# Kernel optimization log

Hardware: AMD Instinct MI355X
Metric: run time of the kernel (lower is better)

The kernel has to match this reference:

```python
import jax, jax.numpy as jnp
import numpy as np
from math import sqrt

NUM_ENT = 100000
NUM_REL = 237  # base; rel table has 2*NUM_REL rows
DIM = 200
HALF = DIM // 2


def _lrelu(x, slope):
    return jnp.where(x >= 0, x, slope * x)


def setup_inputs() -> dict:
    key = jax.random.key(0)
    ks = jax.random.split(key, 20)
    s = 0.02
    inp = {
        'edge_index': jax.random.randint(ks[0], (2, 500000), 0, NUM_ENT),
        'edge_type': jax.random.randint(ks[1], (500000,), 0, 2 * NUM_REL),
        'toTest': jax.random.randint(ks[2], (131072, 2), 0, NUM_ENT),
        'ent_emb': s * jax.random.normal(ks[3], (NUM_ENT, DIM), jnp.float32),
        'rel_emb': s * jax.random.normal(ks[4], (2 * NUM_REL, DIM), jnp.float32),
        'W': s * jax.random.normal(ks[5], (DIM, DIM), jnp.float32),
        'W_loop': s * jax.random.normal(ks[6], (DIM, DIM), jnp.float32),
        'W_rel': s * jax.random.normal(ks[7], (DIM, DIM), jnp.float32),
        'trans_w': s * jax.random.normal(ks[8], (DIM, HALF), jnp.float32),
        'trans_b': jnp.zeros((HALF,), jnp.float32),
        'q_w': s * jax.random.normal(ks[9], (HALF, 128), jnp.float32),
        'q_b': jnp.zeros((128,), jnp.float32),
        'k_w': s * jax.random.normal(ks[10], (HALF, 128), jnp.float32),
        'k_b': jnp.zeros((128,), jnp.float32),
        'w1': s * jax.random.normal(ks[11], (DIM * 2 + 1 + 2 * NUM_REL, 2048), jnp.float32),
        'b1': jnp.zeros((2048,), jnp.float32),
        'w2': s * jax.random.normal(ks[12], (2048, 512), jnp.float32),
        'b2': jnp.zeros((512,), jnp.float32),
        'w3': s * jax.random.normal(ks[13], (512, 1), jnp.float32),
        'b3': jnp.zeros((1,), jnp.float32),
    }
    return inp


def reference(ent_emb, rel_emb, W, W_loop, W_rel, trans_w, trans_b,
              q_w, q_b, k_w, k_b, w1, b1, w2, b2, w3, b3,
              edge_index, edge_type, toTest):
    # --- CompGCN base layer ('sub' composition, degree-normalized scatter-add) ---
    src, dst = edge_index[0], edge_index[1]
    msg = (ent_emb[src] - rel_emb[edge_type]) @ W          # [E, D] gather + GEMM
    deg = jax.ops.segment_sum(jnp.ones_like(dst, jnp.float32), dst, num_segments=NUM_ENT)
    norm = jax.lax.rsqrt(jnp.maximum(deg, 1.0))
    agg = jax.ops.segment_sum(msg, dst, num_segments=NUM_ENT) * norm[:, None]
    all_ent = jnp.tanh(agg + ent_emb @ W_loop)             # [num_ent, D]
    all_rel = rel_emb @ W_rel                              # [2*num_rel, D]

    # --- PairRE test scoring path ---
    head_rel = all_rel[:, :HALF]                           # [2R, D/2]
    tail_rel = all_rel[:, HALF:]
    te = all_ent[toTest]                                   # [N, 2, D] gather
    ee = te @ trans_w + trans_b                            # [N, 2, D/2]
    h_e, t_e = ee[:, 0], ee[:, 1]
    atta = ((h_e @ q_w + q_b) * (t_e @ k_w + k_b)).sum(-1, keepdims=True) / sqrt(DIM)
    relSim = h_e @ head_rel.T - t_e @ tail_rel.T           # [N, 2R]
    cat = jnp.concatenate([te[:, 0], te[:, 1], atta, relSim], axis=1)
    h1 = _lrelu(cat @ w1 + b1, 1e-4)
    h2 = _lrelu(h1 @ w2 + b2, 1e-3)
    return jax.nn.sigmoid(h2 @ w3 + b3)                    # [N, 1]
```

## Files before the change

kernel.cpp:

```cpp
#include <hip/hip_runtime.h>

typedef unsigned short u16;
typedef unsigned long long u64;
typedef __attribute__((ext_vector_type(8))) short bf8;
typedef __attribute__((ext_vector_type(4))) float fx4;

#define N_ENT   100000
#define N_EDGE  500000
#define N_TEST  131072
#define EDIM    200
#define AE_LD   224
#define NB_SCAN 391

__device__ __forceinline__ u16 f2bf(float f) {
  union { float f; unsigned u; } c; c.f = f;
  return (u16)((c.u + 0x7FFFu + ((c.u >> 16) & 1u)) >> 16);
}
__device__ __forceinline__ float bf2f(u16 h) {
  union { unsigned u; float f; } c; c.u = ((unsigned)h) << 16;
  return c.f;
}
__device__ __forceinline__ void gload16(const u16* g, u16* l) {
  __builtin_amdgcn_global_load_lds(
      (const __attribute__((address_space(1))) void*)g,
      (__attribute__((address_space(3))) void*)l, 16, 0, 0);
}

#define BK 32
#define EPS 72

template<int TM, int WN>
__global__ __launch_bounds__(64 * 2 * WN) void gemm_t(
    const u16* __restrict__ A, long lda,
    const u16* __restrict__ B, long ldb,
    u16* __restrict__ out, long ldOut,
    int K,
    const int* __restrict__ rowIdx, int idxMode, int mClamp,
    int mValid, int nValid, int nStore,
    const float* __restrict__ bias, int act, float slope,
    const u16* __restrict__ qbuf, const float* __restrict__ auxF,
    float* __restrict__ dotOut)
{
  constexpr int BM = TM * 32;
  constexpr int BN = WN * 64;
  constexpr int WAVES = 2 * WN;
  __shared__ __align__(16) u16 smem[WAVES * 32 * EPS];
  u16* As = smem;
  u16* Bs = smem + BM * BK;
  const int tid  = threadIdx.x;
  const int wave = tid >> 6, lane = tid & 63;
  const int wr = (wave / WN) * (TM * 16), wc = (wave % WN) * 64;
  const int fr = lane & 15, fq = lane >> 4;
  const long bm = (long)blockIdx.x * BM, bn = (long)blockIdx.y * BN;

  const int srow = wave * 32;
  const int kc = (((lane & 3) ^ ((lane >> 3) & 3)) * 8);
  long a0[2], a1[2], boff[2];
  #pragma unroll
  for (int h = 0; h < 2; ++h) {
    long gmRow = bm + srow + h * 16 + (lane >> 2);
    long b0, b1;
    if (idxMode == 0) {
      long gm = (gmRow >= mClamp) ? (mClamp - 1) : gmRow;
      b0 = gm * lda; b1 = b0;
    } else if (idxMode == 2) {
      b0 = (long)rowIdx[2 * gmRow] * lda; b1 = b0;
    } else if (idxMode == 3) {
      b0 = (long)rowIdx[2 * gmRow + 1] * lda; b1 = b0;
    } else {
      b0 = (long)rowIdx[2 * gmRow] * lda;
      b1 = (long)rowIdx[2 * gmRow + 1] * lda - 224;
    }
    a0[h] = b0 + kc; a1[h] = b1 + kc;
    boff[h] = (bn + srow + h * 16 + (lane >> 2)) * ldb + kc;
  }

  fx4 zero4 = {0.f, 0.f, 0.f, 0.f};
  fx4 acc[TM][4];
  #pragma unroll
  for (int i = 0; i < TM; ++i)
    #pragma unroll
    for (int j = 0; j < 4; ++j) acc[i][j] = zero4;

  for (int k0 = 0; k0 < K; k0 += BK) {
    __syncthreads();
    const bool lo = (k0 + kc) < 224;
    #pragma unroll
    for (int h = 0; h < 2; ++h) {
      const long ao = (idxMode == 4) ? (lo ? a0[h] : a1[h]) : a0[h];
      gload16(A + ao + k0, &As[(srow + h * 16) * BK]);
      gload16(B + boff[h] + k0, &Bs[(srow + h * 16) * BK]);
    }
    __syncthreads();
    bf8 aF[TM], bF[4];
    const int rslot = (fq ^ ((fr >> 1) & 3)) * 8;
    #pragma unroll
    for (int mt = 0; mt < TM; ++mt)
      aF[mt] = *(const bf8*)&As[(wr + mt * 16 + fr) * BK + rslot];
    #pragma unroll
    for (int nt = 0; nt < 4; ++nt)
      bF[nt] = *(const bf8*)&Bs[(wc + nt * 16 + fr) * BK + rslot];
    #pragma unroll
    for (int mt = 0; mt < TM; ++mt)
      #pragma unroll
      for (int nt = 0; nt < 4; ++nt)
        acc[mt][nt] = __builtin_amdgcn_mfma_f32_16x16x32_bf16(aF[mt], bF[nt], acc[mt][nt], 0, 0, 0);
  }

  if (act == 3 || act == 4) {
    #pragma unroll
    for (int mt = 0; mt < TM; ++mt) {
      #pragma unroll
      for (int r = 0; r < 4; ++r) {
        const long gm = bm + wr + mt * 16 + fq * 4 + r;
        float p = 0.f;
        #pragma unroll
        for (int nt = 0; nt < 4; ++nt) {
          const long gn = bn + wc + nt * 16 + fr;
          float v = acc[mt][nt][r] + bias[gn];
          if (act == 3) p += v * bf2f(qbuf[gm * 128 + gn]);
          else { v = (v >= 0.f) ? v : v * slope; p += v * auxF[gn]; }
        }
        p += __shfl_xor(p, 1, 64); p += __shfl_xor(p, 2, 64);
        p += __shfl_xor(p, 4, 64); p += __shfl_xor(p, 8, 64);
        if (fr == 0 && gm < mValid)
          atomicAdd(&dotOut[gm], (act == 3) ? p * 0.07071067811865475f : p);
      }
    }
    return;
  }

  __syncthreads();
  u16* ep = smem + wave * (32 * EPS);
  #pragma unroll
  for (int p = 0; p < TM / 2; ++p) {
    #pragma unroll
    for (int mt2 = 0; mt2 < 2; ++mt2) {
      const int mt = 2 * p + mt2;
      #pragma unroll
      for (int r = 0; r < 4; ++r) {
        const int lrl = mt2 * 16 + fq * 4 + r;
        const long gm = bm + wr + mt * 16 + fq * 4 + r;
        const float attaV = (act == 5) ? dotOut[gm] : 0.f;
        #pragma unroll
        for (int nt = 0; nt < 4; ++nt) {
          const long gn = bn + wc + nt * 16 + fr;
          float v = 0.f;
          if (gn < nValid) {
            v = acc[mt][nt][r];
            if (bias) v += bias[gn];
            if (act == 1) v = tanhf(v);
            else if (act == 5) { v += attaV * auxF[gn]; v = (v >= 0.f) ? v : v * slope; }
          }
          ep[lrl * EPS + nt * 16 + fr] = f2bf(v);
        }
      }
    }
    #pragma unroll
    for (int it = 0; it < 4; ++it) {
      const int lr = it * 8 + (lane >> 3);
      const int lc = (lane & 7) * 8;
      const long gm = bm + wr + p * 32 + lr;
      const long gn = bn + wc + lc;
      if (gm < mValid && gn + 7 < nStore)
        *(bf8*)(out + gm * ldOut + gn) = *(const bf8*)&ep[lr * EPS + lc];
    }
  }
}

__global__ void hist_kernel(const int* __restrict__ ei, int* __restrict__ cnt) {
  int e = blockIdx.x * 256 + threadIdx.x;
  if (e < N_EDGE) atomicAdd(&cnt[ei[N_EDGE + e]], 1);
}
__global__ void scanA_kernel(const int* __restrict__ cnt, int* __restrict__ offs,
                             int* __restrict__ blockSums) {
  __shared__ int s[256];
  int gid = blockIdx.x * 256 + threadIdx.x;
  int v = (gid < N_ENT) ? cnt[gid] : 0;
  s[threadIdx.x] = v;
  __syncthreads();
  for (int off = 1; off < 256; off <<= 1) {
    int t = (threadIdx.x >= off) ? s[threadIdx.x - off] : 0;
    __syncthreads();
    s[threadIdx.x] += t;
    __syncthreads();
  }
  if (gid < N_ENT) offs[gid] = s[threadIdx.x] - v;
  if (threadIdx.x == 255) blockSums[blockIdx.x] = s[255];
}
__global__ void scanB_kernel(const int* __restrict__ blockSums, int* __restrict__ blockOffs) {
  __shared__ int s[512];
  int v = (threadIdx.x < NB_SCAN) ? blockSums[threadIdx.x] : 0;
  s[threadIdx.x] = v;
  __syncthreads();
  for (int off = 1; off < 512; off <<= 1) {
    int t = (threadIdx.x >= off) ? s[threadIdx.x - off] : 0;
    __syncthreads();
    s[threadIdx.x] += t;
    __syncthreads();
  }
  if (threadIdx.x < NB_SCAN) blockOffs[threadIdx.x] = s[threadIdx.x] - v;
}
__global__ void scanC_kernel(int* __restrict__ offs, const int* __restrict__ blockOffs) {
  int gid = blockIdx.x * 256 + threadIdx.x;
  if (gid < N_ENT) offs[gid] += blockOffs[blockIdx.x];
}
__global__ void place_kernel(const int* __restrict__ ei, const int* __restrict__ et,
                             const int* __restrict__ offs, int* __restrict__ cursor,
                             int* __restrict__ sortedSrc, int* __restrict__ sortedT) {
  int e = blockIdx.x * 256 + threadIdx.x;
  if (e >= N_EDGE) return;
  int dst = ei[N_EDGE + e];
  int pos = offs[dst] + atomicAdd(&cursor[dst], 1);
  sortedSrc[pos] = ei[e];
  sortedT[pos]   = et[e];
}
__global__ void agg_A1_kernel(const int* __restrict__ offs, const int* __restrict__ cnt,
                              const int* __restrict__ sortedSrc, const int* __restrict__ sortedT,
                              const float* __restrict__ ent_emb, const float* __restrict__ rel_emb,
                              u16* __restrict__ A1) {
  const int r = blockIdx.x * 4 + (threadIdx.x >> 6);
  if (r >= N_ENT) return;
  const int lane = threadIdx.x & 63;
  const int beg = offs[r], n = cnt[r];
  u16* row = A1 + (size_t)r * 416;
  if (lane < 50) {
    float4 a = {0.f, 0.f, 0.f, 0.f};
    for (int e = 0; e < n; ++e) {
      const int s = sortedSrc[beg + e], t = sortedT[beg + e];
      float4 x = ((const float4*)(ent_emb + (size_t)s * EDIM))[lane];
      float4 y = ((const float4*)(rel_emb + (size_t)t * EDIM))[lane];
      a.x += x.x - y.x; a.y += x.y - y.y; a.z += x.z - y.z; a.w += x.w - y.w;
    }
    const float nm = rsqrtf(fmaxf((float)n, 1.f));
    u64 p = (u64)f2bf(a.x * nm) | ((u64)f2bf(a.y * nm) << 16)
          | ((u64)f2bf(a.z * nm) << 32) | ((u64)f2bf(a.w * nm) << 48);
    *(u64*)(row + 4 * lane) = p;
    float4 e = ((const float4*)(ent_emb + (size_t)r * EDIM))[lane];
    u64 q = (u64)f2bf(e.x) | ((u64)f2bf(e.y) << 16)
          | ((u64)f2bf(e.z) << 32) | ((u64)f2bf(e.w) << 48);
    *(u64*)(row + 200 + 4 * lane) = q;
  }
  if (lane < 16) row[400 + lane] = 0;
}

__global__ void build_B1T(const float* __restrict__ W, const float* __restrict__ W_loop,
                          u16* __restrict__ B1T)
{
  int idx = blockIdx.x * 256 + threadIdx.x;
  if (idx >= 256 * 416) return;
  int n = idx / 416, k = idx % 416;
  float v = 0.f;
  if (n < 200) {
    if (k < 200) v = W[k * 200 + n];
    else if (k < 400) v = W_loop[(k - 200) * 200 + n];
  }
  B1T[idx] = f2bf(v);
}
__global__ void all_rel_kernel(const float* __restrict__ rel_emb, const float* __restrict__ W_rel,
                               float* __restrict__ all_rel)
{
  int r = blockIdx.x, c = threadIdx.x;
  if (c >= 200) return;
  const float* re = rel_emb + r * 200;
  float a = 0.f;
  for (int k = 0; k < 200; ++k) a += re[k] * W_rel[k * 200 + c];
  all_rel[r * 200 + c] = a;
}
__global__ void pq_kernel(const float* __restrict__ all_rel, const float* __restrict__ w1,
                          float* __restrict__ PQ) {
  int idx = blockIdx.x * 256 + threadIdx.x;
  if (idx >= 2 * 100 * 2048) return;
  int n = idx & 2047, m = (idx >> 11) % 100, sel = idx / 204800;
  float a = 0.f;
  for (int r = 0; r < 474; ++r)
    a += all_rel[r * 200 + sel * 100 + m] * w1[(size_t)(401 + r) * 2048 + n];
  PQ[idx] = a;
}
__global__ void p2_kernel(const float* __restrict__ trans_w, const float* __restrict__ PQ,
                          float* __restrict__ P2) {
  int idx = blockIdx.x * 256 + threadIdx.x;
  if (idx >= 2 * 200 * 2048) return;
  int n = idx & 2047, k = (idx >> 11) % 200, sel = idx / 409600;
  const float* pq = PQ + sel * 204800;
  float a = 0.f;
  for (int m = 0; m < 100; ++m) a += trans_w[k * 100 + m] * pq[m * 2048 + n];
  P2[idx] = a;
}
__global__ void w1eff_kernel(const float* __restrict__ w1, const float* __restrict__ P2,
                             u16* __restrict__ W1eff) {
  int idx = blockIdx.x * 256 + threadIdx.x;
  if (idx >= 2048 * 448) return;
  int n = idx / 448, k = idx % 448;
  float v = 0.f;
  if (k < 200) v = w1[(size_t)k * 2048 + n] + P2[(size_t)k * 2048 + n];
  else if (k >= 224 && k < 424) {
    int kk = k - 224;
    v = w1[(size_t)(200 + kk) * 2048 + n] - P2[409600 + (size_t)kk * 2048 + n];
  }
  W1eff[idx] = f2bf(v);
}
__global__ void b1eff_kernel(const float* __restrict__ b1, const float* __restrict__ trans_b,
                             const float* __restrict__ PQ, float* __restrict__ b1eff) {
  int n = blockIdx.x * 256 + threadIdx.x;
  if (n >= 2048) return;
  float a = b1[n];
  for (int m = 0; m < 100; ++m)
    a += trans_b[m] * (PQ[m * 2048 + n] - PQ[204800 + m * 2048 + n]);
  b1eff[n] = a;
}
__global__ void qkw2_kernel(const float* __restrict__ trans_w, const float* __restrict__ q_w,
                            const float* __restrict__ k_w, u16* __restrict__ qw2T,
                            u16* __restrict__ kw2T) {
  int idx = blockIdx.x * 256 + threadIdx.x;
  if (idx >= 128 * 224) return;
  int j = idx / 224, k = idx % 224;
  float a = 0.f, b = 0.f;
  if (k < 200)
    for (int m = 0; m < 100; ++m) {
      float t = trans_w[k * 100 + m];
      a += t * q_w[m * 128 + j];
      b += t * k_w[m * 128 + j];
    }
  qw2T[idx] = f2bf(a);
  kw2T[idx] = f2bf(b);
}
__global__ void qkb2_kernel(const float* __restrict__ q_b, const float* __restrict__ k_b,
                            const float* __restrict__ trans_b, const float* __restrict__ q_w,
                            const float* __restrict__ k_w, float* __restrict__ qb2,
                            float* __restrict__ kb2) {
  int j = threadIdx.x;
  if (j >= 128) return;
  float a = q_b[j], b = k_b[j];
  for (int m = 0; m < 100; ++m) {
    a += trans_b[m] * q_w[m * 128 + j];
    b += trans_b[m] * k_w[m * 128 + j];
  }
  qb2[j] = a; kb2[j] = b;
}
__global__ void build_w2T(const float* __restrict__ w2, u16* __restrict__ w2T)
{
  long idx = (long)blockIdx.x * 256 + threadIdx.x;
  if (idx >= (long)512 * 2048) return;
  int n = (int)(idx / 2048), k = (int)(idx % 2048);
  w2T[idx] = f2bf(w2[(size_t)k * 512 + n]);
}
__global__ void sigmoid_kernel(const float* __restrict__ logit, const float* __restrict__ b3,
                               float* __restrict__ out) {
  int i = blockIdx.x * 256 + threadIdx.x;
  if (i >= N_TEST) return;
  out[i] = 1.f / (1.f + __expf(-(logit[i] + b3[0])));
}

extern "C" void kernel_launch(void* const* d_in, const int* in_sizes, int n_in,
                              void* d_out, int out_size, void* d_ws, size_t ws_size,
                              hipStream_t stream)
{
  (void)in_sizes; (void)n_in; (void)out_size;
  const int*   edge_index = (const int*)d_in[0];
  const int*   edge_type  = (const int*)d_in[1];
  const int*   toTest     = (const int*)d_in[2];
  const float* ent_emb    = (const float*)d_in[3];
  const float* rel_emb    = (const float*)d_in[4];
  const float* W          = (const float*)d_in[5];
  const float* W_loop     = (const float*)d_in[6];
  const float* W_rel      = (const float*)d_in[7];
  const float* trans_w    = (const float*)d_in[8];
  const float* trans_b    = (const float*)d_in[9];
  const float* q_w        = (const float*)d_in[10];
  const float* q_b        = (const float*)d_in[11];
  const float* k_w        = (const float*)d_in[12];
  const float* k_b        = (const float*)d_in[13];
  const float* w1         = (const float*)d_in[14];
  const float* b1         = (const float*)d_in[15];
  const float* w2         = (const float*)d_in[16];
  const float* b2         = (const float*)d_in[17];
  const float* w3         = (const float*)d_in[18];
  const float* b3         = (const float*)d_in[19];
  float* out = (float*)d_out;

  unsigned char* ws = (unsigned char*)d_ws;
  float* atta    = (float*)(ws + 0);
  float* logit   = (float*)(ws + 524288);
  float* allrel  = (float*)(ws + 1048576);
  u16*   B1T     = (u16*)  (ws + 1427968);
  u16*   W1eff   = (u16*)  (ws + 1640960);
  u16*   qw2T    = (u16*)  (ws + 3475968);
  u16*   kw2T    = (u16*)  (ws + 3533312);
  float* b1eff   = (float*)(ws + 3590656);
  float* qb2     = (float*)(ws + 3598848);
  float* kb2     = (float*)(ws + 3599872);
  u16*   w2T     = (u16*)  (ws + 3600896);
  const size_t X_base = 5698048;
  u16*   all_ent = (u16*)  (ws + X_base);
  u16*   Qbuf    = (u16*)  (ws + X_base + 44800000);
  const size_t Y_base = 84052480;
  u16*   A1      = (u16*)  (ws + Y_base);
  const size_t Z_base = 167252480;

  int*   cnt       = (int*)  (ws + Z_base);
  int*   offs      = (int*)  (ws + Z_base + 400000);
  int*   cursor    = (int*)  (ws + Z_base + 800000);
  int*   blockSums = (int*)  (ws + Z_base + 1200000);
  int*   blockOffs = (int*)  (ws + Z_base + 1202048);
  int*   sortedSrc = (int*)  (ws + Z_base + 1204096);
  int*   sortedT   = (int*)  (ws + Z_base + 3204096);
  float* PQ        = (float*)(ws + Z_base + 5204096);
  float* P2        = (float*)(ws + Z_base + 6842496);

  int CH;
  if      (Z_base + (size_t)131072 * 4096 <= ws_size) CH = 131072;
  else if (Z_base + (size_t)65536  * 4096 <= ws_size) CH = 65536;
  else if (Z_base + (size_t)32768  * 4096 <= ws_size) CH = 32768;
  else if (Z_base + (size_t)16384  * 4096 <= ws_size) CH = 16384;
  else if (Z_base + (size_t)8192   * 4096 <= ws_size) CH = 8192;
  else return;
  u16* h1 = (u16*)(ws + Z_base);
  const int NC = N_TEST / CH;

  hipMemsetAsync(cnt, 0, 400000, stream);
  hipMemsetAsync(cursor, 0, 400000, stream);
  hipMemsetAsync(atta, 0, 524288, stream);
  hipMemsetAsync(logit, 0, 524288, stream);

  hist_kernel<<<(N_EDGE + 255) / 256, 256, 0, stream>>>(edge_index, cnt);
  scanA_kernel<<<NB_SCAN, 256, 0, stream>>>(cnt, offs, blockSums);
  scanB_kernel<<<1, 512, 0, stream>>>(blockSums, blockOffs);
  scanC_kernel<<<NB_SCAN, 256, 0, stream>>>(offs, blockOffs);
  place_kernel<<<(N_EDGE + 255) / 256, 256, 0, stream>>>(edge_index, edge_type, offs, cursor,
                                                         sortedSrc, sortedT);
  agg_A1_kernel<<<(N_ENT + 3) / 4, 256, 0, stream>>>(offs, cnt, sortedSrc, sortedT,
                                                     ent_emb, rel_emb, A1);
  build_B1T<<<(256 * 416) / 256, 256, 0, stream>>>(W, W_loop, B1T);

  gemm_t<8, 4><<<dim3(391, 1), 512, 0, stream>>>(A1, 416, B1T, 416, all_ent, AE_LD,
      416, nullptr, 0, N_ENT, N_ENT, 200, AE_LD, nullptr, 1, 0.f, nullptr, nullptr, nullptr);

  all_rel_kernel<<<474, 256, 0, stream>>>(rel_emb, W_rel, allrel);
  pq_kernel<<<(2 * 100 * 2048) / 256, 256, 0, stream>>>(allrel, w1, PQ);
  p2_kernel<<<(2 * 200 * 2048) / 256, 256, 0, stream>>>(trans_w, PQ, P2);
  w1eff_kernel<<<(2048 * 448) / 256, 256, 0, stream>>>(w1, P2, W1eff);
  b1eff_kernel<<<8, 256, 0, stream>>>(b1, trans_b, PQ, b1eff);
  qkw2_kernel<<<(128 * 224) / 256, 256, 0, stream>>>(trans_w, q_w, k_w, qw2T, kw2T);
  qkb2_kernel<<<1, 128, 0, stream>>>(q_b, k_b, trans_b, q_w, k_w, qb2, kb2);
  build_w2T<<<(512 * 2048) / 256, 256, 0, stream>>>(w2, w2T);

  gemm_t<4, 2><<<dim3(1024, 1), 256, 0, stream>>>(all_ent, AE_LD, qw2T, AE_LD, Qbuf, 128,
      AE_LD, toTest, 2, 0, N_TEST, 128, 128, qb2, 0, 0.f, nullptr, nullptr, nullptr);
  gemm_t<4, 2><<<dim3(1024, 1), 256, 0, stream>>>(all_ent, AE_LD, kw2T, AE_LD, nullptr, 0,
      AE_LD, toTest, 3, 0, N_TEST, 128, 128, kb2, 3, 0.f, Qbuf, nullptr, atta);

  for (int c = 0; c < NC; ++c) {
    gemm_t<8, 4><<<dim3(CH / 256, 8), 512, 0, stream>>>(all_ent, AE_LD, W1eff, 448, h1, 2048,
        448, toTest + (size_t)c * CH * 2, 4, 0, CH, 2048, 2048, b1eff, 5, 0.0001f,
        nullptr, w1 + (size_t)400 * 2048, atta + (size_t)c * CH);
    gemm_t<8, 4><<<dim3(CH / 256, 2), 512, 0, stream>>>(h1, 2048, w2T, 2048, nullptr, 0,
        2048, nullptr, 0, CH, CH, 512, 512, b2, 4, 0.001f,
        nullptr, w3, logit + (size_t)c * CH);
  }
  sigmoid_kernel<<<N_TEST / 256, 256, 0, stream>>>(logit, b3, out);
}
```

Baseline: 1.876 ms.

## Double-buffer GEMM LDS tiles and pre-gather test entity rows

The GEMM K-loop now uses two LDS buffers, so the next tile's global-to-LDS load overlaps with the MFMA work on the current tile, and each iteration needs one barrier instead of two. A new gather kernel copies the two indexed entity rows per test pair into a contiguous buffer (reusing the A1 region). The first MLP GEMM can then read plain rows instead of doing indirect two-segment addressing. The maximum chunk size drops to 65536, so the MLP runs as at least two chunks. In exchange, LDS use per block roughly doubles, which may lower occupancy, and the gather adds extra memory traffic.

```diff
diff --git a/kernel.cpp b/kernel.cpp
--- a/kernel.cpp
+++ b/kernel.cpp
@@ -43,10 +43,8 @@
 {
   constexpr int BM = TM * 32;
   constexpr int BN = WN * 64;
-  constexpr int WAVES = 2 * WN;
-  __shared__ __align__(16) u16 smem[WAVES * 32 * EPS];
-  u16* As = smem;
-  u16* Bs = smem + BM * BK;
+  constexpr int BUFS = (BM + BN) * BK;
+  __shared__ __align__(16) u16 smem[2 * BUFS];
   const int tid  = threadIdx.x;
   const int wave = tid >> 6, lane = tid & 63;
   const int wr = (wave / WN) * (TM * 16), wc = (wave % WN) * 64;
@@ -75,6 +73,18 @@
     boff[h] = (bn + srow + h * 16 + (lane >> 2)) * ldb + kc;
   }
 
+  auto STAGE = [&](int buf, int k0) {
+    u16* Ad = smem + buf * BUFS;
+    u16* Bd = Ad + BM * BK;
+    const bool lo = (k0 + kc) < 224;
+    #pragma unroll
+    for (int h = 0; h < 2; ++h) {
+      const long ao = (idxMode == 4) ? (lo ? a0[h] : a1[h]) : a0[h];
+      gload16(A + ao + k0, &Ad[(srow + h * 16) * BK]);
+      gload16(B + boff[h] + k0, &Bd[(srow + h * 16) * BK]);
+    }
+  };
+
   fx4 zero4 = {0.f, 0.f, 0.f, 0.f};
   fx4 acc[TM][4];
   #pragma unroll
@@ -82,29 +92,28 @@
     #pragma unroll
     for (int j = 0; j < 4; ++j) acc[i][j] = zero4;
 
-  for (int k0 = 0; k0 < K; k0 += BK) {
-    __syncthreads();
-    const bool lo = (k0 + kc) < 224;
-    #pragma unroll
-    for (int h = 0; h < 2; ++h) {
-      const long ao = (idxMode == 4) ? (lo ? a0[h] : a1[h]) : a0[h];
-      gload16(A + ao + k0, &As[(srow + h * 16) * BK]);
-      gload16(B + boff[h] + k0, &Bs[(srow + h * 16) * BK]);
-    }
-    __syncthreads();
+  const int NT = K / BK;
+  STAGE(0, 0);
+  __syncthreads();
+  for (int t = 0; t < NT; ++t) {
+    const int cur = t & 1;
+    if (t + 1 < NT) STAGE(cur ^ 1, (t + 1) * BK);
+    const u16* Ac = smem + cur * BUFS;
+    const u16* Bc = Ac + BM * BK;
     bf8 aF[TM], bF[4];
     const int rslot = (fq ^ ((fr >> 1) & 3)) * 8;
     #pragma unroll
     for (int mt = 0; mt < TM; ++mt)
-      aF[mt] = *(const bf8*)&As[(wr + mt * 16 + fr) * BK + rslot];
+      aF[mt] = *(const bf8*)&Ac[(wr + mt * 16 + fr) * BK + rslot];
     #pragma unroll
     for (int nt = 0; nt < 4; ++nt)
-      bF[nt] = *(const bf8*)&Bs[(wc + nt * 16 + fr) * BK + rslot];
+      bF[nt] = *(const bf8*)&Bc[(wc + nt * 16 + fr) * BK + rslot];
     #pragma unroll
     for (int mt = 0; mt < TM; ++mt)
       #pragma unroll
       for (int nt = 0; nt < 4; ++nt)
         acc[mt][nt] = __builtin_amdgcn_mfma_f32_16x16x32_bf16(aF[mt], bF[nt], acc[mt][nt], 0, 0, 0);
+    __syncthreads();
   }
 
   if (act == 3 || act == 4) {
@@ -130,7 +139,6 @@
     return;
   }
 
-  __syncthreads();
   u16* ep = smem + wave * (32 * EPS);
   #pragma unroll
   for (int p = 0; p < TM / 2; ++p) {
@@ -165,6 +173,22 @@
       if (gm < mValid && gn + 7 < nStore)
         *(bf8*)(out + gm * ldOut + gn) = *(const bf8*)&ep[lr * EPS + lc];
     }
+  }
+}
+
+__global__ void gather_te(const int* __restrict__ toTest, const u16* __restrict__ all_ent,
+                          u16* __restrict__ te_cat, int CH) {
+  const int r = blockIdx.x * 4 + (threadIdx.x >> 6);
+  if (r >= CH) return;
+  const int lane = threadIdx.x & 63;
+  u16* dst = te_cat + (size_t)r * 448;
+  if (lane < 28) {
+    const int i0 = toTest[2 * r];
+    *(bf8*)(dst + lane * 8) = *(const bf8*)(all_ent + (size_t)i0 * AE_LD + lane * 8);
+  } else if (lane < 56) {
+    const int i1 = toTest[2 * r + 1];
+    *(bf8*)(dst + 224 + (lane - 28) * 8) =
+        *(const bf8*)(all_ent + (size_t)i1 * AE_LD + (lane - 28) * 8);
   }
 }
 
@@ -409,13 +433,13 @@
   float* P2        = (float*)(ws + Z_base + 6842496);
 
   int CH;
-  if      (Z_base + (size_t)131072 * 4096 <= ws_size) CH = 131072;
-  else if (Z_base + (size_t)65536  * 4096 <= ws_size) CH = 65536;
+  if      (Z_base + (size_t)65536  * 4096 <= ws_size) CH = 65536;
   else if (Z_base + (size_t)32768  * 4096 <= ws_size) CH = 32768;
   else if (Z_base + (size_t)16384  * 4096 <= ws_size) CH = 16384;
   else if (Z_base + (size_t)8192   * 4096 <= ws_size) CH = 8192;
   else return;
-  u16* h1 = (u16*)(ws + Z_base);
+  u16* h1     = (u16*)(ws + Z_base);
+  u16* te_cat = A1;
   const int NC = N_TEST / CH;
 
   hipMemsetAsync(cnt, 0, 400000, stream);
@@ -451,8 +475,9 @@
       AE_LD, toTest, 3, 0, N_TEST, 128, 128, kb2, 3, 0.f, Qbuf, nullptr, atta);
 
   for (int c = 0; c < NC; ++c) {
-    gemm_t<8, 4><<<dim3(CH / 256, 8), 512, 0, stream>>>(all_ent, AE_LD, W1eff, 448, h1, 2048,
-        448, toTest + (size_t)c * CH * 2, 4, 0, CH, 2048, 2048, b1eff, 5, 0.0001f,
+    gather_te<<<CH / 4, 256, 0, stream>>>(toTest + (size_t)c * CH * 2, all_ent, te_cat, CH);
+    gemm_t<8, 4><<<dim3(CH / 256, 8), 512, 0, stream>>>(te_cat, 448, W1eff, 448, h1, 2048,
+        448, nullptr, 0, CH, CH, 2048, 2048, b1eff, 5, 0.0001f,
         nullptr, w1 + (size_t)400 * 2048, atta + (size_t)c * CH);
     gemm_t<8, 4><<<dim3(CH / 256, 2), 512, 0, stream>>>(h1, 2048, w2T, 2048, nullptr, 0,
         2048, nullptr, 0, CH, CH, 512, 512, b2, 4, 0.001f,
```

Result: slower. 1.948 ms (+3.8%).
